# Performance work log

Hardware: AMD Instinct MI355X
Metric: run time of the kernel (lower is better)

The kernel has to match this reference:

```python
import jax, jax.numpy as jnp
import numpy as np
import math

S, E, D, H = 4096, 512, 64, 8  # sentence_length, imbd_size, hidden_size, num_heads


def setup_inputs() -> dict:
    key = jax.random.key(0)
    k1, k2, k3, k4, k5 = jax.random.split(key, 5)
    return {
        "X": jax.random.normal(k1, (S, E), dtype=jnp.float32),
        "W_q": jax.random.uniform(k2, (H, E, D), dtype=jnp.float32),
        "W_k": jax.random.uniform(k3, (H, E, D), dtype=jnp.float32),
        "W_v": jax.random.uniform(k4, (H, E, D), dtype=jnp.float32),
        "W_0": jax.random.uniform(k5, (E, D), dtype=jnp.float32),
    }


def reference(X, W_q, W_k, W_v, W_0):
    # Per-head projections: X [S,E] broadcast across heads -> [H,S,D]
    q = jnp.einsum('se,hed->hsd', X, W_q)
    k = jnp.einsum('se,hed->hsd', X, W_k)
    v = jnp.einsum('se,hed->hsd', X, W_v)
    # Scaled scores [H,S,S]; softmax over keys (last axis), no mask
    scores = jnp.einsum('hsd,htd->hst', q, k) / math.sqrt(D)
    attn = jax.nn.softmax(scores, axis=-1)
    r3 = jnp.einsum('hst,htd->hsd', attn, v)  # [H,S,D]
    # Concat heads: permute to [S,H,D] -> [S,H*D], then output proj [E,D]
    Z = r3.transpose(1, 0, 2).reshape(S, H * D) @ W_0  # [S,D]
    return Z
```

## Files before the change

kernel.cpp:

```cpp
#include <hip/hip_runtime.h>
#include <hip/hip_bf16.h>

#define S_LEN 4096
#define E_DIM 512
#define D_DIM 64
#define H_NUM 8
#define KSPLIT 4
#define NKT ((S_LEN / KSPLIT) / 64)
#define QSCALE 0.18033688011112042f

typedef short bf16x8 __attribute__((ext_vector_type(8)));
typedef float f32x4 __attribute__((ext_vector_type(4)));
typedef unsigned short u16x8 __attribute__((ext_vector_type(8)));
typedef unsigned short u16x4 __attribute__((ext_vector_type(4)));

__device__ inline unsigned short f2bf(float x) {
    union { float f; unsigned u; } v; v.f = x;
    unsigned r = v.u + 0x7FFFu + ((v.u >> 16) & 1u);
    return (unsigned short)(r >> 16);
}
__device__ inline float bf2f(unsigned short b) {
    union { unsigned u; float f; } v; v.u = ((unsigned)b) << 16;
    return v.f;
}
__device__ inline f32x4 mfma16(bf16x8 a, bf16x8 b, f32x4 c) {
    return __builtin_amdgcn_mfma_f32_16x16x32_bf16(a, b, c, 0, 0, 0);
}
__device__ inline void gl_lds16(const void* g, void* l) {
    __builtin_amdgcn_global_load_lds(
        (const __attribute__((address_space(1))) void*)g,
        (__attribute__((address_space(3))) void*)l, 16, 0, 0);
}
__device__ inline unsigned cvtpk(float a, float b) {
    unsigned r;
    asm volatile("v_cvt_pk_bf16_f32 %0, %1, %2" : "=v"(r) : "v"(a), "v"(b));
    return r;
}

__global__ __launch_bounds__(256) void prepass_kernel(
    const float* __restrict__ X, const float* __restrict__ Wq,
    const float* __restrict__ Wk, const float* __restrict__ Wv,
    unsigned short* __restrict__ Xhi, unsigned short* __restrict__ Xlo,
    unsigned short* __restrict__ WT)
{
    int bx = blockIdx.x;
    if (bx < 2048) {
        int i = (bx * 256 + threadIdx.x) * 4;
        float4 v = *(const float4*)&X[i];
        float a[4] = {v.x, v.y, v.z, v.w};
        u16x4 hv, lv;
#pragma unroll
        for (int j = 0; j < 4; ++j) {
            unsigned short hb = f2bf(a[j]);
            hv[j] = hb;
            lv[j] = f2bf(a[j] - bf2f(hb));
        }
        *(u16x4*)&Xhi[i] = hv;
        *(u16x4*)&Xlo[i] = lv;
    } else {
        int wid = bx - 2048;
        int z = wid >> 8;
        const float* W = (z == 0) ? Wq : (z == 1) ? Wk : Wv;
        int idx = (wid & 255) * 256 + threadIdx.x;
        int n = idx >> 7;
        int e = (idx & 127) * 4;
        int hh = n >> 6, d = n & 63;
        unsigned short* Whi = WT + (size_t)z * 2 * 262144;
        unsigned short* Wlo = Whi + 262144;
        u16x4 hv, lv;
#pragma unroll
        for (int j = 0; j < 4; ++j) {
            float v = W[((size_t)hh * E_DIM + e + j) * D_DIM + d];
            unsigned short hb = f2bf(v);
            hv[j] = hb;
            lv[j] = f2bf(v - bf2f(hb));
        }
        *(u16x4*)&Whi[(size_t)n * E_DIM + e] = hv;
        *(u16x4*)&Wlo[(size_t)n * E_DIM + e] = lv;
    }
}

__global__ __launch_bounds__(256) void proj_kernel(
    const unsigned short* __restrict__ Xhi, const unsigned short* __restrict__ Xlo,
    const unsigned short* __restrict__ WT,
    unsigned short* __restrict__ Qhi, unsigned short* __restrict__ Qlo,
    unsigned short* __restrict__ Khi, unsigned short* __restrict__ Klo,
    unsigned short* __restrict__ Vt)
{
    __shared__ __align__(16) unsigned short XhS[128 * 64];
    __shared__ __align__(16) unsigned short XlS[128 * 64];
    __shared__ __align__(16) unsigned short WhS[128 * 64];
    __shared__ __align__(16) unsigned short WlS[128 * 64];

    const int s0 = blockIdx.x * 128, n0 = blockIdx.y * 128, z = blockIdx.z;
    const unsigned short* Wh_g = WT + (size_t)z * 524288;
    const unsigned short* Wl_g = Wh_g + 262144;

    const int tid = threadIdx.x, lane = tid & 63, w = tid >> 6;
    const int l15 = lane & 15, lhi = lane >> 4;
    const int wr = w >> 1, wc = w & 1;

    const int chunk = lane & 7;
    size_t aoff[4], boff[4];
    int ldso[4];
#pragma unroll
    for (int i = 0; i < 4; ++i) {
        int r = w * 32 + i * 8 + (lane >> 3);
        int swz = (chunk * 16) ^ ((r & 7) << 4);
        aoff[i] = ((size_t)(s0 + r)) * 1024 + swz;
        boff[i] = ((size_t)(n0 + r)) * 1024 + swz;
        ldso[i] = (w * 32 + i * 8) * 128;
    }

    f32x4 acc[4][4];
#pragma unroll
    for (int a = 0; a < 4; ++a)
#pragma unroll
        for (int b = 0; b < 4; ++b) acc[a][b] = (f32x4){0.f, 0.f, 0.f, 0.f};

    for (int kb = 0; kb < E_DIM; kb += 64) {
        __syncthreads();
#pragma unroll
        for (int i = 0; i < 4; ++i) {
            size_t ab = aoff[i] + kb * 2;
            size_t bb = boff[i] + kb * 2;
            gl_lds16((const char*)Xhi + ab, (char*)XhS + ldso[i]);
            gl_lds16((const char*)Xlo + ab, (char*)XlS + ldso[i]);
            gl_lds16((const char*)Wh_g + bb, (char*)WhS + ldso[i]);
            gl_lds16((const char*)Wl_g + bb, (char*)WlS + ldso[i]);
        }
        __syncthreads();

#pragma unroll
        for (int kc = 0; kc < 2; ++kc) {
            int cb = kc * 64 + lhi * 16;
            bf16x8 ah[4], al[4], bh[4], bl[4];
#pragma unroll
            for (int rt = 0; rt < 4; ++rt) {
                int row = wr * 64 + rt * 16 + l15;
                int ad = row * 128 + (cb ^ ((row & 7) << 4));
                ah[rt] = *(const bf16x8*)((const char*)XhS + ad);
                al[rt] = *(const bf16x8*)((const char*)XlS + ad);
            }
#pragma unroll
            for (int nt = 0; nt < 4; ++nt) {
                int n = wc * 64 + nt * 16 + l15;
                int bd = n * 128 + (cb ^ ((n & 7) << 4));
                bh[nt] = *(const bf16x8*)((const char*)WhS + bd);
                bl[nt] = *(const bf16x8*)((const char*)WlS + bd);
            }
#pragma unroll
            for (int rt = 0; rt < 4; ++rt)
#pragma unroll
                for (int nt = 0; nt < 4; ++nt) {
                    acc[rt][nt] = mfma16(ah[rt], bh[nt], acc[rt][nt]);
                    acc[rt][nt] = mfma16(ah[rt], bl[nt], acc[rt][nt]);
                    acc[rt][nt] = mfma16(al[rt], bh[nt], acc[rt][nt]);
                }
        }
    }

#pragma unroll
    for (int rt = 0; rt < 4; ++rt)
#pragma unroll
        for (int nt = 0; nt < 4; ++nt) {
            int n = n0 + wc * 64 + nt * 16 + l15;
            int hh = n >> 6, d = n & 63;
            if (z == 2) {
                u16x4 vv;
#pragma unroll
                for (int j = 0; j < 4; ++j) vv[j] = f2bf(acc[rt][nt][j]);
                int sb = s0 + wr * 64 + rt * 16 + lhi * 4;
                *(u16x4*)&Vt[((size_t)(hh * D_DIM + d)) * S_LEN + sb] = vv;
            } else {
#pragma unroll
                for (int j = 0; j < 4; ++j) {
                    int s = s0 + wr * 64 + rt * 16 + lhi * 4 + j;
                    float val = acc[rt][nt][j];
                    size_t o = ((size_t)hh * S_LEN + s) * D_DIM + d;
                    if (z == 0) {
                        val *= QSCALE;
                        unsigned short hb = f2bf(val);
                        Qhi[o] = hb;
                        Qlo[o] = f2bf(val - bf2f(hb));
                    } else {
                        unsigned short hb = f2bf(val);
                        Khi[o] = hb;
                        Klo[o] = f2bf(val - bf2f(hb));
                    }
                }
            }
        }
}

__global__ __launch_bounds__(256) void flash_kernel(
    const unsigned short* __restrict__ Qhi, const unsigned short* __restrict__ Qlo,
    const unsigned short* __restrict__ Khi_g, const unsigned short* __restrict__ Klo_g,
    const unsigned short* __restrict__ Vt_g,
    unsigned short* __restrict__ Part, float2* __restrict__ ML)
{
    __shared__ __align__(16) char lds[2][24576];
    __shared__ __align__(16) unsigned short PS[4][16 * 64];

    const int h  = blockIdx.y;
    const int ks = blockIdx.z;
    const int q0 = blockIdx.x * 64;
    const int tid  = threadIdx.x;
    const int lane = tid & 63;
    const int w    = tid >> 6;
    const int l15  = lane & 15;
    const int lhi  = lane >> 4;

    const int qrow = q0 + w * 16 + l15;
    bf16x8 qh[2], ql[2];
#pragma unroll
    for (int c = 0; c < 2; ++c) {
        size_t off = ((size_t)(h * S_LEN + qrow)) * D_DIM + lhi * 8 + 32 * c;
        qh[c] = *(const bf16x8*)&Qhi[off];
        ql[c] = *(const bf16x8*)&Qlo[off];
    }

    const char *pKh[2], *pKl[2], *pV[2];
    int ldsd[2];
    {
        const int chunk = lane & 7;
#pragma unroll
        for (int i = 0; i < 2; ++i) {
            int r = w * 16 + i * 8 + (lane >> 3);
            int swz = (chunk * 16) ^ ((r & 7) << 4);
            size_t kb = ((size_t)(h * S_LEN + ks * (S_LEN / KSPLIT) + r)) * 128 + swz;
            pKh[i] = (const char*)Khi_g + kb;
            pKl[i] = (const char*)Klo_g + kb;
            size_t vb = ((size_t)(h * D_DIM + r) * S_LEN + ks * (S_LEN / KSPLIT)) * 2 + swz;
            pV[i] = (const char*)Vt_g + vb;
            ldsd[i] = (w * 16 + i * 8) * 128;
        }
    }

#define STAGE(B) do {                                            \
        _Pragma("unroll")                                        \
        for (int i = 0; i < 2; ++i) {                            \
            char* base = &lds[(B)][0];                           \
            gl_lds16(pKh[i], base + ldsd[i]);                    \
            gl_lds16(pKl[i], base + 8192 + ldsd[i]);             \
            gl_lds16(pV[i],  base + 16384 + ldsd[i]);            \
            pKh[i] += 8192; pKl[i] += 8192; pV[i] += 128;        \
        }                                                        \
    } while (0)

    f32x4 acc_o[4];
#pragma unroll
    for (int nt = 0; nt < 4; ++nt) acc_o[nt] = (f32x4){0.f, 0.f, 0.f, 0.f};
    float m2 = -1e30f, lsum = 0.f;

    unsigned short* pw = &PS[w][0];

    STAGE(0);
    __syncthreads();

    int buf = 0;
    for (int kt = 0; kt < NKT; ++kt) {
        if (kt + 1 < NKT) STAGE(buf ^ 1);

        const char* Kh = &lds[buf][0];
        const char* Kl = Kh + 8192;
        const char* Vl = Kh + 16384;

        f32x4 sacc[4];
#pragma unroll
        for (int nt = 0; nt < 4; ++nt) sacc[nt] = (f32x4){0.f, 0.f, 0.f, 0.f};
        __builtin_amdgcn_s_setprio(1);
#pragma unroll
        for (int c = 0; c < 2; ++c) {
            int colb = (lhi * 8 + 32 * c) * 2;
#pragma unroll
            for (int nt = 0; nt < 4; ++nt) {
                int key = l15 + 16 * nt;
                int lo = key * 128 + (((colb >> 4) ^ (key & 7)) << 4);
                bf16x8 kh = *(const bf16x8*)(Kh + lo);
                bf16x8 kl = *(const bf16x8*)(Kl + lo);
                sacc[nt] = mfma16(kh, qh[c], sacc[nt]);
                sacc[nt] = mfma16(kl, qh[c], sacc[nt]);
                sacc[nt] = mfma16(kh, ql[c], sacc[nt]);
            }
        }
        __builtin_amdgcn_s_setprio(0);

        float mx0 = fmaxf(fmaxf(sacc[0][0], sacc[0][1]), fmaxf(sacc[0][2], sacc[0][3]));
        float mx1 = fmaxf(fmaxf(sacc[1][0], sacc[1][1]), fmaxf(sacc[1][2], sacc[1][3]));
        float mx2 = fmaxf(fmaxf(sacc[2][0], sacc[2][1]), fmaxf(sacc[2][2], sacc[2][3]));
        float mx3 = fmaxf(fmaxf(sacc[3][0], sacc[3][1]), fmaxf(sacc[3][2], sacc[3][3]));
        float vm = fmaxf(fmaxf(mx0, mx1), fmaxf(mx2, mx3));
        vm = fmaxf(vm, __shfl_xor(vm, 16));
        vm = fmaxf(vm, __shfl_xor(vm, 32));

        if (!__all(vm <= m2 + 8.f)) {
            float mnew = fmaxf(m2, vm);
            float sc = exp2f(m2 - mnew);
            m2 = mnew;
            lsum *= sc;
            float scj[4];
#pragma unroll
            for (int j = 0; j < 4; ++j) scj[j] = __shfl(sc, lhi * 4 + j);
#pragma unroll
            for (int nt = 0; nt < 4; ++nt)
#pragma unroll
                for (int j = 0; j < 4; ++j) acc_o[nt][j] *= scj[j];
        }

        float sum = 0.f;
#pragma unroll
        for (int nt = 0; nt < 4; ++nt) {
            float e0 = exp2f(sacc[nt][0] - m2);
            float e1 = exp2f(sacc[nt][1] - m2);
            float e2 = exp2f(sacc[nt][2] - m2);
            float e3 = exp2f(sacc[nt][3] - m2);
            sum += (e0 + e1) + (e2 + e3);
            int colb = 32 * nt + 8 * lhi;
            int adr = l15 * 128 + ((((colb >> 4)) ^ (l15 & 7)) << 4) + (colb & 15);
            uint2 pk = make_uint2(cvtpk(e0, e1), cvtpk(e2, e3));
            *(uint2*)((char*)pw + adr) = pk;
        }
        sum += __shfl_xor(sum, 16);
        sum += __shfl_xor(sum, 32);
        lsum += sum;

        __builtin_amdgcn_s_setprio(1);
#pragma unroll
        for (int c = 0; c < 2; ++c) {
            int colb = (lhi * 8 + 32 * c) * 2;
            int loA = l15 * 128 + (((colb >> 4) ^ (l15 & 7)) << 4);
            bf16x8 pa = *(const bf16x8*)((const char*)pw + loA);
#pragma unroll
            for (int nt = 0; nt < 4; ++nt) {
                int d = l15 + 16 * nt;
                int loB = d * 128 + (((colb >> 4) ^ (d & 7)) << 4);
                bf16x8 vb = *(const bf16x8*)(Vl + loB);
                acc_o[nt] = mfma16(pa, vb, acc_o[nt]);
            }
        }
        __builtin_amdgcn_s_setprio(0);

        if (kt + 1 < NKT) {
            __syncthreads();
            buf ^= 1;
        }
    }
#undef STAGE

    if (lane < 16) {
        ML[(size_t)(ks * H_NUM + h) * S_LEN + q0 + w * 16 + l15] =
            make_float2(m2, lsum);
    }
    unsigned short* PT = Part + ((size_t)(ks * H_NUM + h)) * S_LEN * D_DIM;
#pragma unroll
    for (int r = 0; r < 4; ++r) {
        float lr = __shfl(lsum, lhi * 4 + r);
        float inv = 1.f / lr;
        int s = q0 + w * 16 + lhi * 4 + r;
#pragma unroll
        for (int nt = 0; nt < 4; ++nt)
            PT[(size_t)s * D_DIM + l15 + 16 * nt] = f2bf(acc_o[nt][r] * inv);
    }
}

__global__ __launch_bounds__(256) void cw_kernel(
    const float2* __restrict__ ML, float4* __restrict__ CW)
{
    int i = blockIdx.x * 256 + threadIdx.x;
    float2 a[KSPLIT];
    float m = -1e30f;
#pragma unroll
    for (int k = 0; k < KSPLIT; ++k) {
        a[k] = ML[(size_t)k * H_NUM * S_LEN + i];
        m = fmaxf(m, a[k].x);
    }
    float wk[KSPLIT], wsum = 0.f;
#pragma unroll
    for (int k = 0; k < KSPLIT; ++k) {
        wk[k] = exp2f(a[k].x - m) * a[k].y;
        wsum += wk[k];
    }
    float inv = 1.f / wsum;
    CW[i] = make_float4(wk[0] * inv, wk[1] * inv, wk[2] * inv, wk[3] * inv);
}

__global__ __launch_bounds__(256) void zout_kernel(
    const unsigned short* __restrict__ Part, const float4* __restrict__ CW,
    const float* __restrict__ W0, float* __restrict__ Z)
{
    __shared__ __align__(16) float Rs[32][64];
    __shared__ __align__(16) float Ws[32][64];

    const size_t PSZ = (size_t)H_NUM * S_LEN * D_DIM;
    const int s0 = blockIdx.x * 64;
    const int tid = threadIdx.x;
    const int tx = tid & 15;
    const int ty = tid >> 4;

    float acc[4][4];
#pragma unroll
    for (int i = 0; i < 4; ++i)
#pragma unroll
        for (int j = 0; j < 4; ++j) acc[i][j] = 0.f;

    for (int kb = 0; kb < E_DIM; kb += 32) {
        __syncthreads();
#pragma unroll
        for (int p = 0; p < 2; ++p) {
            int idx = tid + 256 * p;
            int row = idx >> 3;
            int kq  = idx & 7;
            int k = kb + kq * 4;
            int hh = k >> 6, d0 = k & 63;
            int s = s0 + row;
            size_t pbase = ((size_t)hh * S_LEN + s) * D_DIM + d0;
            float4 c = *(const float4*)&CW[hh * S_LEN + s];
            u16x4 a0 = *(const u16x4*)&Part[pbase];
            u16x4 a1 = *(const u16x4*)&Part[PSZ + pbase];
            u16x4 a2 = *(const u16x4*)&Part[2 * PSZ + pbase];
            u16x4 a3 = *(const u16x4*)&Part[3 * PSZ + pbase];
#pragma unroll
            for (int j = 0; j < 4; ++j)
                Rs[kq * 4 + j][row] = bf2f(a0[j]) * c.x + bf2f(a1[j]) * c.y +
                                      bf2f(a2[j]) * c.z + bf2f(a3[j]) * c.w;
        }
#pragma unroll
        for (int p = 0; p < 2; ++p) {
            int idx = tid + 256 * p;
            int k  = idx >> 4;
            int nq = idx & 15;
            *(float4*)&Ws[k][nq * 4] = *(const float4*)&W0[(size_t)(kb + k) * D_DIM + nq * 4];
        }
        __syncthreads();

#pragma unroll 8
        for (int k = 0; k < 32; ++k) {
            float a[4], b[4];
            *(float4*)&a[0] = *(const float4*)&Rs[k][ty * 4];
            *(float4*)&b[0] = *(const float4*)&Ws[k][tx * 4];
#pragma unroll
            for (int i = 0; i < 4; ++i)
#pragma unroll
                for (int j = 0; j < 4; ++j) acc[i][j] += a[i] * b[j];
        }
    }

#pragma unroll
    for (int i = 0; i < 4; ++i) {
        float4 o = make_float4(acc[i][0], acc[i][1], acc[i][2], acc[i][3]);
        *(float4*)&Z[(size_t)(s0 + ty * 4 + i) * D_DIM + tx * 4] = o;
    }
}

extern "C" void kernel_launch(void* const* d_in, const int* in_sizes, int n_in,
                              void* d_out, int out_size, void* d_ws, size_t ws_size,
                              hipStream_t stream) {
    const float* X  = (const float*)d_in[0];
    const float* Wq = (const float*)d_in[1];
    const float* Wk = (const float*)d_in[2];
    const float* Wv = (const float*)d_in[3];
    const float* W0 = (const float*)d_in[4];

    char* ws = (char*)d_ws;
    const size_t MB = 1ull << 20;
    unsigned short* Qhi = (unsigned short*)(ws + 0 * MB);
    unsigned short* Qlo = (unsigned short*)(ws + 4 * MB);
    unsigned short* Khi = (unsigned short*)(ws + 8 * MB);
    unsigned short* Klo = (unsigned short*)(ws + 12 * MB);
    unsigned short* Vt  = (unsigned short*)(ws + 16 * MB);
    unsigned short* Xhi = (unsigned short*)(ws + 24 * MB);
    unsigned short* Xlo = (unsigned short*)(ws + 28 * MB);
    unsigned short* WT  = (unsigned short*)(ws + 32 * MB);
    unsigned short* Part = (unsigned short*)(ws + 20 * MB);
    float2* ML = (float2*)(ws + 36 * MB);
    float4* CW = (float4*)(ws + 37 * MB);

    float* Z = (float*)d_out;

    prepass_kernel<<<dim3(2048 + 768), 256, 0, stream>>>(X, Wq, Wk, Wv, Xhi, Xlo, WT);
    proj_kernel<<<dim3(S_LEN / 128, 4, 3), 256, 0, stream>>>(
        Xhi, Xlo, WT, Qhi, Qlo, Khi, Klo, Vt);
    flash_kernel<<<dim3(S_LEN / 64, H_NUM, KSPLIT), 256, 0, stream>>>(
        Qhi, Qlo, Khi, Klo, Vt, Part, ML);
    cw_kernel<<<dim3(H_NUM * S_LEN / 256), 256, 0, stream>>>(ML, CW);
    zout_kernel<<<dim3(S_LEN / 64), 256, 0, stream>>>(Part, CW, W0, Z);
}
```

Baseline: 246.7 us.

## Process two query tiles per flash block, drop K/V double buffering

Each flash block now handles 128 query rows (two 64-row groups per wave set) against every staged K/V tile, so each K/V load into LDS is reused twice and the grid halves. The double-buffered LDS staging is replaced with a single buffer bracketed by two barriers per iteration. This cuts global-to-LDS traffic but raises register pressure (doubled accumulators and Q fragments) and loses the overlap between loads and compute. With fewer blocks, occupancy across CUs may also drop.

```diff
diff --git a/kernel.cpp b/kernel.cpp
--- a/kernel.cpp
+++ b/kernel.cpp
@@ -199,25 +199,28 @@
     const unsigned short* __restrict__ Vt_g,
     unsigned short* __restrict__ Part, float2* __restrict__ ML)
 {
-    __shared__ __align__(16) char lds[2][24576];
-    __shared__ __align__(16) unsigned short PS[4][16 * 64];
+    __shared__ __align__(16) char lds[24576];
+    __shared__ __align__(16) unsigned short PS[4][2][16 * 64];
 
     const int h  = blockIdx.y;
     const int ks = blockIdx.z;
-    const int q0 = blockIdx.x * 64;
+    const int q0 = blockIdx.x * 128;
     const int tid  = threadIdx.x;
     const int lane = tid & 63;
     const int w    = tid >> 6;
     const int l15  = lane & 15;
     const int lhi  = lane >> 4;
 
-    const int qrow = q0 + w * 16 + l15;
-    bf16x8 qh[2], ql[2];
-#pragma unroll
-    for (int c = 0; c < 2; ++c) {
-        size_t off = ((size_t)(h * S_LEN + qrow)) * D_DIM + lhi * 8 + 32 * c;
-        qh[c] = *(const bf16x8*)&Qhi[off];
-        ql[c] = *(const bf16x8*)&Qlo[off];
+    bf16x8 qh[2][2], ql[2][2];
+#pragma unroll
+    for (int g = 0; g < 2; ++g) {
+        const int qrow = q0 + g * 64 + w * 16 + l15;
+#pragma unroll
+        for (int c = 0; c < 2; ++c) {
+            size_t off = ((size_t)(h * S_LEN + qrow)) * D_DIM + lhi * 8 + 32 * c;
+            qh[g][c] = *(const bf16x8*)&Qhi[off];
+            ql[g][c] = *(const bf16x8*)&Qlo[off];
+        }
     }
 
     const char *pKh[2], *pKl[2], *pV[2];
@@ -237,38 +240,34 @@
         }
     }
 
-#define STAGE(B) do {                                            \
-        _Pragma("unroll")                                        \
-        for (int i = 0; i < 2; ++i) {                            \
-            char* base = &lds[(B)][0];                           \
-            gl_lds16(pKh[i], base + ldsd[i]);                    \
-            gl_lds16(pKl[i], base + 8192 + ldsd[i]);             \
-            gl_lds16(pV[i],  base + 16384 + ldsd[i]);            \
-            pKh[i] += 8192; pKl[i] += 8192; pV[i] += 128;        \
-        }                                                        \
-    } while (0)
-
-    f32x4 acc_o[4];
-#pragma unroll
-    for (int nt = 0; nt < 4; ++nt) acc_o[nt] = (f32x4){0.f, 0.f, 0.f, 0.f};
-    float m2 = -1e30f, lsum = 0.f;
-
-    unsigned short* pw = &PS[w][0];
-
-    STAGE(0);
-    __syncthreads();
-
-    int buf = 0;
+    f32x4 acc_o[2][4];
+#pragma unroll
+    for (int g = 0; g < 2; ++g)
+#pragma unroll
+        for (int nt = 0; nt < 4; ++nt) acc_o[g][nt] = (f32x4){0.f, 0.f, 0.f, 0.f};
+    float m2[2] = {-1e30f, -1e30f};
+    float lsum[2] = {0.f, 0.f};
+
     for (int kt = 0; kt < NKT; ++kt) {
-        if (kt + 1 < NKT) STAGE(buf ^ 1);
-
-        const char* Kh = &lds[buf][0];
-        const char* Kl = Kh + 8192;
-        const char* Vl = Kh + 16384;
-
-        f32x4 sacc[4];
-#pragma unroll
-        for (int nt = 0; nt < 4; ++nt) sacc[nt] = (f32x4){0.f, 0.f, 0.f, 0.f};
+        __syncthreads();
+#pragma unroll
+        for (int i = 0; i < 2; ++i) {
+            gl_lds16(pKh[i], lds + ldsd[i]);
+            gl_lds16(pKl[i], lds + 8192 + ldsd[i]);
+            gl_lds16(pV[i],  lds + 16384 + ldsd[i]);
+            pKh[i] += 8192; pKl[i] += 8192; pV[i] += 128;
+        }
+        __syncthreads();
+
+        const char* Kh = lds;
+        const char* Kl = lds + 8192;
+        const char* Vl = lds + 16384;
+
+        f32x4 sacc[2][4];
+#pragma unroll
+        for (int g = 0; g < 2; ++g)
+#pragma unroll
+            for (int nt = 0; nt < 4; ++nt) sacc[g][nt] = (f32x4){0.f, 0.f, 0.f, 0.f};
         __builtin_amdgcn_s_setprio(1);
 #pragma unroll
         for (int c = 0; c < 2; ++c) {
@@ -279,88 +278,94 @@
                 int lo = key * 128 + (((colb >> 4) ^ (key & 7)) << 4);
                 bf16x8 kh = *(const bf16x8*)(Kh + lo);
                 bf16x8 kl = *(const bf16x8*)(Kl + lo);
-                sacc[nt] = mfma16(kh, qh[c], sacc[nt]);
-                sacc[nt] = mfma16(kl, qh[c], sacc[nt]);
-                sacc[nt] = mfma16(kh, ql[c], sacc[nt]);
+#pragma unroll
+                for (int g = 0; g < 2; ++g) {
+                    sacc[g][nt] = mfma16(kh, qh[g][c], sacc[g][nt]);
+                    sacc[g][nt] = mfma16(kl, qh[g][c], sacc[g][nt]);
+                    sacc[g][nt] = mfma16(kh, ql[g][c], sacc[g][nt]);
+                }
             }
         }
         __builtin_amdgcn_s_setprio(0);
 
-        float mx0 = fmaxf(fmaxf(sacc[0][0], sacc[0][1]), fmaxf(sacc[0][2], sacc[0][3]));
-        float mx1 = fmaxf(fmaxf(sacc[1][0], sacc[1][1]), fmaxf(sacc[1][2], sacc[1][3]));
-        float mx2 = fmaxf(fmaxf(sacc[2][0], sacc[2][1]), fmaxf(sacc[2][2], sacc[2][3]));
-        float mx3 = fmaxf(fmaxf(sacc[3][0], sacc[3][1]), fmaxf(sacc[3][2], sacc[3][3]));
-        float vm = fmaxf(fmaxf(mx0, mx1), fmaxf(mx2, mx3));
-        vm = fmaxf(vm, __shfl_xor(vm, 16));
-        vm = fmaxf(vm, __shfl_xor(vm, 32));
-
-        if (!__all(vm <= m2 + 8.f)) {
-            float mnew = fmaxf(m2, vm);
-            float sc = exp2f(m2 - mnew);
-            m2 = mnew;
-            lsum *= sc;
-            float scj[4];
-#pragma unroll
-            for (int j = 0; j < 4; ++j) scj[j] = __shfl(sc, lhi * 4 + j);
-#pragma unroll
-            for (int nt = 0; nt < 4; ++nt)
-#pragma unroll
-                for (int j = 0; j < 4; ++j) acc_o[nt][j] *= scj[j];
-        }
-
-        float sum = 0.f;
-#pragma unroll
-        for (int nt = 0; nt < 4; ++nt) {
-            float e0 = exp2f(sacc[nt][0] - m2);
-            float e1 = exp2f(sacc[nt][1] - m2);
-            float e2 = exp2f(sacc[nt][2] - m2);
-            float e3 = exp2f(sacc[nt][3] - m2);
-            sum += (e0 + e1) + (e2 + e3);
-            int colb = 32 * nt + 8 * lhi;
-            int adr = l15 * 128 + ((((colb >> 4)) ^ (l15 & 7)) << 4) + (colb & 15);
-            uint2 pk = make_uint2(cvtpk(e0, e1), cvtpk(e2, e3));
-            *(uint2*)((char*)pw + adr) = pk;
-        }
-        sum += __shfl_xor(sum, 16);
-        sum += __shfl_xor(sum, 32);
-        lsum += sum;
+#pragma unroll
+        for (int g = 0; g < 2; ++g) {
+            float mx0 = fmaxf(fmaxf(sacc[g][0][0], sacc[g][0][1]), fmaxf(sacc[g][0][2], sacc[g][0][3]));
+            float mx1 = fmaxf(fmaxf(sacc[g][1][0], sacc[g][1][1]), fmaxf(sacc[g][1][2], sacc[g][1][3]));
+            float mx2 = fmaxf(fmaxf(sacc[g][2][0], sacc[g][2][1]), fmaxf(sacc[g][2][2], sacc[g][2][3]));
+            float mx3 = fmaxf(fmaxf(sacc[g][3][0], sacc[g][3][1]), fmaxf(sacc[g][3][2], sacc[g][3][3]));
+            float vm = fmaxf(fmaxf(mx0, mx1), fmaxf(mx2, mx3));
+            vm = fmaxf(vm, __shfl_xor(vm, 16));
+            vm = fmaxf(vm, __shfl_xor(vm, 32));
+
+            if (!__all(vm <= m2[g] + 8.f)) {
+                float mnew = fmaxf(m2[g], vm);
+                float sc = exp2f(m2[g] - mnew);
+                m2[g] = mnew;
+                lsum[g] *= sc;
+                float scj[4];
+#pragma unroll
+                for (int j = 0; j < 4; ++j) scj[j] = __shfl(sc, lhi * 4 + j);
+#pragma unroll
+                for (int nt = 0; nt < 4; ++nt)
+#pragma unroll
+                    for (int j = 0; j < 4; ++j) acc_o[g][nt][j] *= scj[j];
+            }
+
+            float sum = 0.f;
+            unsigned short* pw = &PS[w][g][0];
+#pragma unroll
+            for (int nt = 0; nt < 4; ++nt) {
+                float e0 = exp2f(sacc[g][nt][0] - m2[g]);
+                float e1 = exp2f(sacc[g][nt][1] - m2[g]);
+                float e2 = exp2f(sacc[g][nt][2] - m2[g]);
+                float e3 = exp2f(sacc[g][nt][3] - m2[g]);
+                sum += (e0 + e1) + (e2 + e3);
+                int colb = 32 * nt + 8 * lhi;
+                int adr = l15 * 128 + ((((colb >> 4)) ^ (l15 & 7)) << 4) + (colb & 15);
+                uint2 pk = make_uint2(cvtpk(e0, e1), cvtpk(e2, e3));
+                *(uint2*)((char*)pw + adr) = pk;
+            }
+            sum += __shfl_xor(sum, 16);
+            sum += __shfl_xor(sum, 32);
+            lsum[g] += sum;
+        }
 
         __builtin_amdgcn_s_setprio(1);
 #pragma unroll
         for (int c = 0; c < 2; ++c) {
             int colb = (lhi * 8 + 32 * c) * 2;
             int loA = l15 * 128 + (((colb >> 4) ^ (l15 & 7)) << 4);
-            bf16x8 pa = *(const bf16x8*)((const char*)pw + loA);
+            bf16x8 pa0 = *(const bf16x8*)((const char*)&PS[w][0][0] + loA);
+            bf16x8 pa1 = *(const bf16x8*)((const char*)&PS[w][1][0] + loA);
 #pragma unroll
             for (int nt = 0; nt < 4; ++nt) {
                 int d = l15 + 16 * nt;
                 int loB = d * 128 + (((colb >> 4) ^ (d & 7)) << 4);
                 bf16x8 vb = *(const bf16x8*)(Vl + loB);
-                acc_o[nt] = mfma16(pa, vb, acc_o[nt]);
+                acc_o[0][nt] = mfma16(pa0, vb, acc_o[0][nt]);
+                acc_o[1][nt] = mfma16(pa1, vb, acc_o[1][nt]);
             }
         }
         __builtin_amdgcn_s_setprio(0);
-
-        if (kt + 1 < NKT) {
-            __syncthreads();
-            buf ^= 1;
-        }
-    }
-#undef STAGE
-
-    if (lane < 16) {
-        ML[(size_t)(ks * H_NUM + h) * S_LEN + q0 + w * 16 + l15] =
-            make_float2(m2, lsum);
-    }
+    }
+
     unsigned short* PT = Part + ((size_t)(ks * H_NUM + h)) * S_LEN * D_DIM;
 #pragma unroll
-    for (int r = 0; r < 4; ++r) {
-        float lr = __shfl(lsum, lhi * 4 + r);
-        float inv = 1.f / lr;
-        int s = q0 + w * 16 + lhi * 4 + r;
-#pragma unroll
-        for (int nt = 0; nt < 4; ++nt)
-            PT[(size_t)s * D_DIM + l15 + 16 * nt] = f2bf(acc_o[nt][r] * inv);
+    for (int g = 0; g < 2; ++g) {
+        if (lane < 16) {
+            ML[(size_t)(ks * H_NUM + h) * S_LEN + q0 + g * 64 + w * 16 + l15] =
+                make_float2(m2[g], lsum[g]);
+        }
+#pragma unroll
+        for (int r = 0; r < 4; ++r) {
+            float lr = __shfl(lsum[g], lhi * 4 + r);
+            float inv = 1.f / lr;
+            int s = q0 + g * 64 + w * 16 + lhi * 4 + r;
+#pragma unroll
+            for (int nt = 0; nt < 4; ++nt)
+                PT[(size_t)s * D_DIM + l15 + 16 * nt] = f2bf(acc_o[g][nt][r] * inv);
+        }
     }
 }
 
@@ -481,7 +486,7 @@
     prepass_kernel<<<dim3(2048 + 768), 256, 0, stream>>>(X, Wq, Wk, Wv, Xhi, Xlo, WT);
     proj_kernel<<<dim3(S_LEN / 128, 4, 3), 256, 0, stream>>>(
         Xhi, Xlo, WT, Qhi, Qlo, Khi, Klo, Vt);
-    flash_kernel<<<dim3(S_LEN / 64, H_NUM, KSPLIT), 256, 0, stream>>>(
+    flash_kernel<<<dim3(S_LEN / 128, H_NUM, KSPLIT), 256, 0, stream>>>(
         Qhi, Qlo, Khi, Klo, Vt, Part, ML);
     cw_kernel<<<dim3(H_NUM * S_LEN / 256), 256, 0, stream>>>(ML, CW);
     zout_kernel<<<dim3(S_LEN / 64), 256, 0, stream>>>(Part, CW, W0, Z);
```

New measurement: 229.2 us. 1.08x faster.
